# Kernel tuning notes

Measured on AMD Instinct MI355X. Metric: run time of the kernel, lower is better.

Reference implementation:

```python
import jax, jax.numpy as jnp
import numpy as np

EMB = 2048
HEADS = 16
HEAD_DIM = EMB // HEADS
LATENT = 512
B, S = 2, 2048


def setup_inputs() -> dict:
    key = jax.random.key(0)
    ks = jax.random.split(key, 7)
    sc = lambda fan_in: 1.0 / np.sqrt(fan_in)
    return {
        "x": jax.random.normal(ks[0], (B, S, EMB), dtype=jnp.float32),
        "w_q": jax.random.normal(ks[1], (EMB, EMB), dtype=jnp.float32) * sc(EMB),
        "w_down": jax.random.normal(ks[2], (LATENT, EMB), dtype=jnp.float32) * sc(EMB),
        "w_up_k": jax.random.normal(ks[3], (EMB, LATENT), dtype=jnp.float32) * sc(LATENT),
        "w_up_v": jax.random.normal(ks[4], (EMB, LATENT), dtype=jnp.float32) * sc(LATENT),
        "w_out": jax.random.normal(ks[5], (EMB, EMB), dtype=jnp.float32) * sc(EMB),
        "b_out": jax.random.normal(ks[6], (EMB,), dtype=jnp.float32) * 0.01,
    }


def reference(x, w_q, w_down, w_up_k, w_up_v, w_out, b_out):
    # Linear uses torch convention: y = x @ W.T
    q = jnp.einsum("bse,fe->bsf", x, w_q)          # [B,S,EMB]
    latent = jnp.einsum("bse,le->bsl", x, w_down)  # [B,S,LATENT]
    k = jnp.einsum("bsl,fl->bsf", latent, w_up_k)
    v = jnp.einsum("bsl,fl->bsf", latent, w_up_v)

    def heads(t):  # [B,S,EMB] -> [B,H,S,D]
        return t.reshape(B, S, HEADS, HEAD_DIM).transpose(0, 2, 1, 3)

    qh, kh, vh = heads(q), heads(k), heads(v)
    scores = jnp.einsum("bhqd,bhkd->bhqk", qh, kh)  # [B,H,S,S]
    qpos = jnp.arange(S)
    causal = qpos[:, None] < qpos[None, :]          # True where future (masked)
    scores = jnp.where(causal[None, None], -jnp.inf, scores)
    attn = jax.nn.softmax(scores / np.sqrt(HEAD_DIM).astype(np.float32), axis=-1)
    ctx = jnp.einsum("bhqk,bhkd->bhqd", attn, vh)   # [B,H,S,D]
    ctx = ctx.transpose(0, 2, 1, 3).reshape(B, S, EMB)
    return jnp.einsum("bse,fe->bsf", ctx, w_out) + b_out
```

## Files before the change

kernel.cpp:

```cpp
#include <hip/hip_runtime.h>
#include <hip/hip_bf16.h>

#define EMB 2048
#define HEADS 16
#define HDIM 128
#define LATENT 512
#define BATCH 2
#define SEQ 2048
#define MROWS (BATCH*SEQ)

typedef __attribute__((ext_vector_type(4))) float f32x4;
typedef __attribute__((ext_vector_type(8))) short s16x8;

__device__ __forceinline__ unsigned short f2bf(float f) {
  __hip_bfloat16 h = __float2bfloat16(f);
  union { __hip_bfloat16 h; unsigned short u; } c; c.h = h; return c.u;
}

#define GLOAD_LDS16(g, l) \
  __builtin_amdgcn_global_load_lds((const __attribute__((address_space(1))) unsigned int*)(g), \
                                   (__attribute__((address_space(3))) unsigned int*)(l), 16, 0, 0)

__global__ void cvt_kernel(const float* __restrict__ src, unsigned short* __restrict__ dst, int n4) {
  int i = blockIdx.x * blockDim.x + threadIdx.x;
  int stride = gridDim.x * blockDim.x;
  for (; i < n4; i += stride) {
    float4 v = reinterpret_cast<const float4*>(src)[i];
    ushort4 o;
    o.x = f2bf(v.x); o.y = f2bf(v.y); o.z = f2bf(v.z); o.w = f2bf(v.w);
    reinterpret_cast<ushort4*>(dst)[i] = o;
  }
}

#define BM 128
#define BN 128
#define BK 32

template<int OUTF32>
__global__ __launch_bounds__(256) void gemm_bt(
    const unsigned short* __restrict__ A, const unsigned short* __restrict__ B,
    void* __restrict__ C, const float* __restrict__ bias, int M, int N, int K)
{
  __shared__ __align__(16) unsigned short sA[BM][BK];
  __shared__ __align__(16) unsigned short sB[BN][BK];
  const int tid  = threadIdx.x;
  const int lane = tid & 63, wave = tid >> 6;
  const int wm = wave >> 1, wn = wave & 1;
  const int lrow = lane & 15, kgrp = lane >> 4;

  const int gx = gridDim.x;
  const int nwg = gx * gridDim.y;
  const int orig = blockIdx.y * gx + blockIdx.x;
  const int chunk = nwg >> 3;
  const int sw = (orig & 7) * chunk + (orig >> 3);
  const long bm = (long)(sw / gx) * BM, bn = (long)(sw % gx) * BN;

  const int srow = tid >> 2;
  const int scol = (tid & 3) * 8;

  f32x4 zero4 = {0.f, 0.f, 0.f, 0.f};
  f32x4 acc[4][4];
  #pragma unroll
  for (int i = 0; i < 4; ++i)
    #pragma unroll
    for (int j = 0; j < 4; ++j) acc[i][j] = zero4;

  const unsigned short* ga = A + (bm + srow) * (long)K + scol;
  const unsigned short* gb = B + (bn + srow) * (long)K + scol;

  for (int k0 = 0; k0 < K; k0 += BK) {
    GLOAD_LDS16(ga + k0,                 &sA[srow][scol]);
    GLOAD_LDS16(ga + 64*(long)K + k0,    &sA[srow + 64][scol]);
    GLOAD_LDS16(gb + k0,                 &sB[srow][scol]);
    GLOAD_LDS16(gb + 64*(long)K + k0,    &sB[srow + 64][scol]);
    __syncthreads();

    s16x8 aF[4], bF[4];
    #pragma unroll
    for (int i = 0; i < 4; ++i) {
      aF[i] = *reinterpret_cast<const s16x8*>(&sA[wm*64 + i*16 + lrow][kgrp*8]);
      bF[i] = *reinterpret_cast<const s16x8*>(&sB[wn*64 + i*16 + lrow][kgrp*8]);
    }
    #pragma unroll
    for (int i = 0; i < 4; ++i)
      #pragma unroll
      for (int j = 0; j < 4; ++j)
        acc[i][j] = __builtin_amdgcn_mfma_f32_16x16x32_bf16(aF[i], bF[j], acc[i][j], 0, 0, 0);
    __syncthreads();
  }

  #pragma unroll
  for (int i = 0; i < 4; ++i) {
    #pragma unroll
    for (int j = 0; j < 4; ++j) {
      long row = bm + wm*64 + i*16 + kgrp*4;
      long col = bn + wn*64 + j*16 + lrow;
      if (OUTF32) {
        float* Cf = (float*)C;
        float bv = bias[col];
        #pragma unroll
        for (int r = 0; r < 4; ++r) Cf[(row + r) * (long)N + col] = acc[i][j][r] + bv;
      } else {
        unsigned short* Cb = (unsigned short*)C;
        #pragma unroll
        for (int r = 0; r < 4; ++r) Cb[(row + r) * (long)N + col] = f2bf(acc[i][j][r]);
      }
    }
  }
}

#define G2_LDS (96*1024)

template<int OUTF32>
__global__ __launch_bounds__(512, 1) void gemm256(
    const unsigned short* __restrict__ A, const unsigned short* __restrict__ B,
    void* __restrict__ C, const float* __restrict__ bias, int M, int N, int K)
{
  extern __shared__ char smem[];
  const int tid  = threadIdx.x;
  const int lane = tid & 63, wave = tid >> 6;
  const int wm = wave >> 1, wn = wave & 1;
  const int lrow = lane & 15, kgrp = lane >> 4;

  const int gx = gridDim.x;
  const int nwg = gx * gridDim.y;
  const int orig = blockIdx.y * gx + blockIdx.x;
  const int chunk = nwg >> 3;
  const int sw = (orig & 7) * chunk + (orig >> 3);
  const long bm = (long)(sw / gx) * 256, bn = (long)(sw % gx) * 128;

  const int strow = tid >> 3;
  const int scolB = ((tid & 7) * 16) ^ ((strow & 7) << 4);
  const unsigned short* gaS = A + (bm + strow) * (long)K + (scolB >> 1);
  const unsigned short* gbS = B + (bn + strow) * (long)K + (scolB >> 1);

  int fcol[2];
  #pragma unroll
  for (int kh = 0; kh < 2; ++kh) fcol[kh] = (kh * 64 + kgrp * 16) ^ ((lrow & 7) << 4);

  f32x4 zero4 = {0.f, 0.f, 0.f, 0.f};
  f32x4 acc[4][4];
  #pragma unroll
  for (int i = 0; i < 4; ++i)
    #pragma unroll
    for (int j = 0; j < 4; ++j) acc[i][j] = zero4;

  const int NT = K >> 6;
  auto stage = [&](int cur, int t) {
    const long k0 = (long)t * 64;
    unsigned short* sa = (unsigned short*)(smem) + cur * 16384 + tid * 8;
    unsigned short* sb = (unsigned short*)(smem + 65536) + cur * 8192 + tid * 8;
    #pragma unroll
    for (int R = 0; R < 4; ++R) GLOAD_LDS16(gaS + (R * 64) * (long)K + k0, sa + R * 4096);
    #pragma unroll
    for (int R = 0; R < 2; ++R) GLOAD_LDS16(gbS + (R * 64) * (long)K + k0, sb + R * 4096);
  };

  stage(0, 0);
  __syncthreads();

  int cur = 0;
  for (int t = 0; t < NT; ++t) {
    if (t + 1 < NT) stage(cur ^ 1, t + 1);
    const char* sa = smem + cur * 32768;
    const char* sb = smem + 65536 + cur * 16384;
    #pragma unroll
    for (int kh = 0; kh < 2; ++kh) {
      s16x8 aF[4], bF[4];
      #pragma unroll
      for (int i = 0; i < 4; ++i)
        aF[i] = *reinterpret_cast<const s16x8*>(sa + (wm*64 + i*16 + lrow) * 128 + fcol[kh]);
      #pragma unroll
      for (int j = 0; j < 4; ++j)
        bF[j] = *reinterpret_cast<const s16x8*>(sb + (wn*64 + j*16 + lrow) * 128 + fcol[kh]);
      __builtin_amdgcn_s_setprio(1);
      #pragma unroll
      for (int i = 0; i < 4; ++i)
        #pragma unroll
        for (int j = 0; j < 4; ++j)
          acc[i][j] = __builtin_amdgcn_mfma_f32_16x16x32_bf16(aF[i], bF[j], acc[i][j], 0, 0, 0);
      __builtin_amdgcn_s_setprio(0);
    }
    __syncthreads();
    cur ^= 1;
  }

  #pragma unroll
  for (int i = 0; i < 4; ++i) {
    #pragma unroll
    for (int j = 0; j < 4; ++j) {
      long row = bm + wm*64 + i*16 + kgrp*4;
      long col = bn + wn*64 + j*16 + lrow;
      if (OUTF32) {
        float* Cf = (float*)C;
        float bv = bias[col];
        #pragma unroll
        for (int r = 0; r < 4; ++r) Cf[(row + r) * (long)N + col] = acc[i][j][r] + bv;
      } else {
        unsigned short* Cb = (unsigned short*)C;
        #pragma unroll
        for (int r = 0; r < 4; ++r) Cb[(row + r) * (long)N + col] = f2bf(acc[i][j][r]);
      }
    }
  }
}

#define KVB 64
#define QTB 64
#define NQT3 (SEQ/QTB)

__global__ __launch_bounds__(256, 2) void attn4_kernel(
    const unsigned short* __restrict__ Q, const unsigned short* __restrict__ Kg,
    const unsigned short* __restrict__ Vt, unsigned short* __restrict__ CTX)
{
  const int bid = blockIdx.x;
  const int rest = bid >> 3;
  const int pr = rest & 15;
  const int g = (bid & 7) + 8 * (rest >> 4);
  const int h = g & 15, b = g >> 4;

  const int tid = threadIdx.x, w = tid >> 6, lane = tid & 63;
  const int lrow = lane & 15, kgrp = lane >> 4;
  const size_t bS = (size_t)b * SEQ;

  __shared__ __align__(16) unsigned short sK[2][KVB * HDIM];
  __shared__ __align__(16) unsigned short sP[4][16][72];

  const int krow  = tid >> 4;
  const int kcolB = ((tid & 15) * 16) ^ (((tid >> 4) & 7) << 4);
  const unsigned short* kst_g = Kg + (bS + krow) * EMB + h * HDIM + (kcolB >> 1);

  const int swz = (lrow & 7) << 4;
  int cc[4];
  #pragma unroll
  for (int kk = 0; kk < 4; ++kk) cc[kk] = ((kk * 64 + kgrp * 16) ^ swz) >> 1;

  const float C = 0.12751742f;
  const float THR = 11.5f;
  f32x4 zero4 = {0.f, 0.f, 0.f, 0.f};
  s16x8 onesF;
  #pragma unroll
  for (int i = 0; i < 8; ++i) onesF[i] = (short)0x3F80;

  const int qts[2] = {NQT3 - 1 - pr, pr};
  for (int ps = 0; ps < 2; ++ps) {
    const int qt = qts[ps];
    const int nt = qt + 1;
    const int qw = qt * QTB + w * 16;

    s16x8 qF[4];
    #pragma unroll
    for (int kk = 0; kk < 4; ++kk)
      qF[kk] = *reinterpret_cast<const s16x8*>(
          Q + (bS + qw + lrow) * EMB + h * HDIM + kk * 32 + kgrp * 8);

    f32x4 o[8];
    #pragma unroll
    for (int dt = 0; dt < 8; ++dt) o[dt] = zero4;
    float rm[4], rl[4];
    #pragma unroll
    for (int r = 0; r < 4; ++r) { rm[r] = -1.0e30f; rl[r] = 0.f; }

    __syncthreads();
    {
      unsigned short* l0 = &sK[0][0] + tid * 8;
      #pragma unroll
      for (int R = 0; R < 4; ++R) GLOAD_LDS16(kst_g + (size_t)R * 16 * EMB, l0 + R * 2048);
    }

    for (int j = 0; j < nt; ++j) {
      __syncthreads();
      const int kv0 = j * KVB;
      if (j + 1 < nt) {
        const unsigned short* gs = kst_g + (size_t)(j + 1) * KVB * EMB;
        unsigned short* ls = &sK[(j + 1) & 1][0] + tid * 8;
        #pragma unroll
        for (int R = 0; R < 4; ++R) GLOAD_LDS16(gs + (size_t)R * 16 * EMB, ls + R * 2048);
      }

      s16x8 vF[2][8];
      #pragma unroll
      for (int hf = 0; hf < 2; ++hf)
        #pragma unroll
        for (int dt = 0; dt < 8; ++dt)
          vF[hf][dt] = *reinterpret_cast<const s16x8*>(
              Vt + (size_t)(h * HDIM + dt * 16 + lrow) * MROWS + bS + kv0 + hf * 32 + kgrp * 8);

      const unsigned short* kb = &sK[j & 1][0];
      f32x4 sc[4];
      #pragma unroll
      for (int kvg = 0; kvg < 4; ++kvg) sc[kvg] = zero4;
      __builtin_amdgcn_s_setprio(1);
      #pragma unroll
      for (int kvg = 0; kvg < 4; ++kvg) {
        const int rb = (kvg * 16 + lrow) * HDIM;
        #pragma unroll
        for (int kk = 0; kk < 4; ++kk) {
          s16x8 kF = *reinterpret_cast<const s16x8*>(kb + rb + cc[kk]);
          sc[kvg] = __builtin_amdgcn_mfma_f32_16x16x32_bf16(qF[kk], kF, sc[kvg], 0, 0, 0);
        }
      }
      __builtin_amdgcn_s_setprio(0);

      const bool needm = (kv0 + 63 > qw);
      float sv[4][4];
      #pragma unroll
      for (int kvg = 0; kvg < 4; ++kvg)
        #pragma unroll
        for (int r = 0; r < 4; ++r) {
          float s = sc[kvg][r];
          if (needm) {
            int qq  = qw + kgrp * 4 + r;
            int col = kv0 + kvg * 16 + lrow;
            s = (col <= qq) ? s : -3.0e38f;
          }
          sv[kvg][r] = s;
        }
      float tm[4];
      #pragma unroll
      for (int r = 0; r < 4; ++r)
        tm[r] = fmaxf(fmaxf(sv[0][r], sv[1][r]), fmaxf(sv[2][r], sv[3][r]));
      #pragma unroll
      for (int m = 1; m < 16; m <<= 1)
        #pragma unroll
        for (int r = 0; r < 4; ++r) tm[r] = fmaxf(tm[r], __shfl_xor(tm[r], m));

      float d = tm[0] * C - rm[0];
      #pragma unroll
      for (int r = 1; r < 4; ++r) d = fmaxf(d, tm[r] * C - rm[r]);
      const bool skip = __all(d <= THR);

      float mn[4];
      #pragma unroll
      for (int r = 0; r < 4; ++r) mn[r] = skip ? rm[r] : fmaxf(rm[r], tm[r] * C);

      #pragma unroll
      for (int r = 0; r < 4; ++r) {
        float p0 = exp2f(fmaf(sv[0][r], C, -mn[r]));
        float p1 = exp2f(fmaf(sv[1][r], C, -mn[r]));
        float p2 = exp2f(fmaf(sv[2][r], C, -mn[r]));
        float p3 = exp2f(fmaf(sv[3][r], C, -mn[r]));
        const int qrow = kgrp * 4 + r;
        sP[w][qrow][ 0 + lrow] = f2bf(p0);
        sP[w][qrow][16 + lrow] = f2bf(p1);
        sP[w][qrow][32 + lrow] = f2bf(p2);
        sP[w][qrow][48 + lrow] = f2bf(p3);
      }
      if (!skip) {
        #pragma unroll
        for (int r = 0; r < 4; ++r) {
          float corr = exp2f(rm[r] - mn[r]);
          rm[r] = mn[r];
          rl[r] *= corr;
          #pragma unroll
          for (int dt = 0; dt < 8; ++dt) o[dt][r] *= corr;
        }
      }

      s16x8 pF[2];
      #pragma unroll
      for (int hf = 0; hf < 2; ++hf)
        pF[hf] = *reinterpret_cast<const s16x8*>(&sP[w][lrow][hf * 32 + kgrp * 8]);
      f32x4 psum = zero4;
      __builtin_amdgcn_s_setprio(1);
      psum = __builtin_amdgcn_mfma_f32_16x16x32_bf16(pF[0], onesF, psum, 0, 0, 0);
      psum = __builtin_amdgcn_mfma_f32_16x16x32_bf16(pF[1], onesF, psum, 0, 0, 0);
      #pragma unroll
      for (int dt = 0; dt < 8; ++dt) {
        o[dt] = __builtin_amdgcn_mfma_f32_16x16x32_bf16(pF[0], vF[0][dt], o[dt], 0, 0, 0);
        o[dt] = __builtin_amdgcn_mfma_f32_16x16x32_bf16(pF[1], vF[1][dt], o[dt], 0, 0, 0);
      }
      __builtin_amdgcn_s_setprio(0);
      #pragma unroll
      for (int r = 0; r < 4; ++r) rl[r] += psum[r];
    }

    float iv[4];
    #pragma unroll
    for (int r = 0; r < 4; ++r) iv[r] = 1.0f / rl[r];
    #pragma unroll
    for (int dt = 0; dt < 8; ++dt)
      #pragma unroll
      for (int r = 0; r < 4; ++r)
        CTX[(bS + qw + kgrp * 4 + r) * EMB + h * HDIM + dt * 16 + lrow] =
            f2bf(o[dt][r] * iv[r]);
  }
}

extern "C" void kernel_launch(void* const* d_in, const int* in_sizes, int n_in,
                              void* d_out, int out_size, void* d_ws, size_t ws_size,
                              hipStream_t stream)
{
  const float* x      = (const float*)d_in[0];
  const float* w_q    = (const float*)d_in[1];
  const float* w_down = (const float*)d_in[2];
  const float* w_upk  = (const float*)d_in[3];
  const float* w_upv  = (const float*)d_in[4];
  const float* w_out  = (const float*)d_in[5];
  const float* b_out  = (const float*)d_in[6];
  float* out = (float*)d_out;

  static bool attr_done = false;
  if (!attr_done) {
    hipFuncSetAttribute((const void*)gemm256<0>, hipFuncAttributeMaxDynamicSharedMemorySize, G2_LDS);
    hipFuncSetAttribute((const void*)gemm256<1>, hipFuncAttributeMaxDynamicSharedMemorySize, G2_LDS);
    attr_done = true;
  }

  char* ws = (char*)d_ws;
  size_t off = 0;
  auto alloc = [&](size_t elems) {
    void* p = ws + off; off += elems * 2; off = (off + 255) & ~(size_t)255; return p;
  };
  unsigned short* xb   = (unsigned short*)alloc((size_t)MROWS * EMB);
  unsigned short* wqb  = (unsigned short*)alloc((size_t)EMB * EMB);
  unsigned short* wdb  = (unsigned short*)alloc((size_t)LATENT * EMB);
  unsigned short* wkb  = (unsigned short*)alloc((size_t)EMB * LATENT);
  unsigned short* wvb  = (unsigned short*)alloc((size_t)EMB * LATENT);
  unsigned short* wob  = (unsigned short*)alloc((size_t)EMB * EMB);
  unsigned short* qb   = (unsigned short*)alloc((size_t)MROWS * EMB);
  unsigned short* latb = (unsigned short*)alloc((size_t)MROWS * LATENT);
  unsigned short* kb   = (unsigned short*)alloc((size_t)MROWS * EMB);
  unsigned short* vtb  = (unsigned short*)alloc((size_t)EMB * MROWS);
  unsigned short* ctxb = xb;

  auto cvt = [&](const float* s, unsigned short* d, size_t n) {
    int n4 = (int)(n / 4);
    int blocks = (n4 + 255) / 256; if (blocks > 1024) blocks = 1024;
    cvt_kernel<<<dim3(blocks), dim3(256), 0, stream>>>(s, d, n4);
  };
  cvt(x,      xb,  (size_t)MROWS * EMB);
  cvt(w_q,    wqb, (size_t)EMB * EMB);
  cvt(w_down, wdb, (size_t)LATENT * EMB);
  cvt(w_upk,  wkb, (size_t)EMB * LATENT);
  cvt(w_upv,  wvb, (size_t)EMB * LATENT);
  cvt(w_out,  wob, (size_t)EMB * EMB);

  gemm256<0><<<dim3(EMB/128, MROWS/256), 512, G2_LDS, stream>>>(xb, wqb, qb, nullptr, MROWS, EMB, EMB);
  gemm_bt<0><<<dim3(LATENT/BN, MROWS/BM), 256, 0, stream>>>(xb, wdb, latb, nullptr, MROWS, LATENT, EMB);
  gemm256<0><<<dim3(EMB/128, MROWS/256), 512, G2_LDS, stream>>>(latb, wkb, kb, nullptr, MROWS, EMB, LATENT);
  gemm256<0><<<dim3(MROWS/128, EMB/256), 512, G2_LDS, stream>>>(wvb, latb, vtb, nullptr, EMB, MROWS, LATENT);

  attn4_kernel<<<dim3(512, 1, 1), 256, 0, stream>>>(qb, kb, vtb, ctxb);

  gemm256<1><<<dim3(EMB/128, MROWS/256), 512, G2_LDS, stream>>>(ctxb, wob, (void*)out, b_out, MROWS, EMB, EMB);
}
```

Measured before the change: 411.1 us.

## Compute transposed S tile so each lane owns one query row in softmax

Swaps the MFMA operand order for the QK^T product so scores come out transposed, with each lane holding one query row across 16 kv positions. The row max and sum then need only two cross-lane shuffles instead of a four-step butterfly on four values each. The row-sum MFMAs against a ones vector are replaced by a scalar accumulation. P is written to LDS as packed 32-bit stores. In exchange, the rescale factor and the final reciprocal must be shuffled back into the O accumulator layout, which adds a few extra shuffles.

```diff
diff --git a/kernel.cpp b/kernel.cpp
--- a/kernel.cpp
+++ b/kernel.cpp
@@ -209,7 +209,7 @@
 #define QTB 64
 #define NQT3 (SEQ/QTB)
 
-__global__ __launch_bounds__(256, 2) void attn4_kernel(
+__global__ __launch_bounds__(256, 2) void attn5_kernel(
     const unsigned short* __restrict__ Q, const unsigned short* __restrict__ Kg,
     const unsigned short* __restrict__ Vt, unsigned short* __restrict__ CTX)
 {
@@ -221,6 +221,7 @@
 
   const int tid = threadIdx.x, w = tid >> 6, lane = tid & 63;
   const int lrow = lane & 15, kgrp = lane >> 4;
+  const int qloc = lrow;
   const size_t bS = (size_t)b * SEQ;
 
   __shared__ __align__(16) unsigned short sK[2][KVB * HDIM];
@@ -238,15 +239,13 @@
   const float C = 0.12751742f;
   const float THR = 11.5f;
   f32x4 zero4 = {0.f, 0.f, 0.f, 0.f};
-  s16x8 onesF;
-  #pragma unroll
-  for (int i = 0; i < 8; ++i) onesF[i] = (short)0x3F80;
 
   const int qts[2] = {NQT3 - 1 - pr, pr};
   for (int ps = 0; ps < 2; ++ps) {
     const int qt = qts[ps];
     const int nt = qt + 1;
     const int qw = qt * QTB + w * 16;
+    const int q_abs = qw + qloc;
 
     s16x8 qF[4];
     #pragma unroll
@@ -257,9 +256,7 @@
     f32x4 o[8];
     #pragma unroll
     for (int dt = 0; dt < 8; ++dt) o[dt] = zero4;
-    float rm[4], rl[4];
-    #pragma unroll
-    for (int r = 0; r < 4; ++r) { rm[r] = -1.0e30f; rl[r] = 0.f; }
+    float rm = -1.0e30f, rl = 0.f;
 
     __syncthreads();
     {
@@ -297,7 +294,7 @@
         #pragma unroll
         for (int kk = 0; kk < 4; ++kk) {
           s16x8 kF = *reinterpret_cast<const s16x8*>(kb + rb + cc[kk]);
-          sc[kvg] = __builtin_amdgcn_mfma_f32_16x16x32_bf16(qF[kk], kF, sc[kvg], 0, 0, 0);
+          sc[kvg] = __builtin_amdgcn_mfma_f32_16x16x32_bf16(kF, qF[kk], sc[kvg], 0, 0, 0);
         }
       }
       __builtin_amdgcn_s_setprio(0);
@@ -310,74 +307,78 @@
         for (int r = 0; r < 4; ++r) {
           float s = sc[kvg][r];
           if (needm) {
-            int qq  = qw + kgrp * 4 + r;
-            int col = kv0 + kvg * 16 + lrow;
-            s = (col <= qq) ? s : -3.0e38f;
+            int kv = kv0 + kvg * 16 + kgrp * 4 + r;
+            s = (kv <= q_abs) ? s : -3.0e38f;
           }
           sv[kvg][r] = s;
         }
-      float tm[4];
-      #pragma unroll
-      for (int r = 0; r < 4; ++r)
-        tm[r] = fmaxf(fmaxf(sv[0][r], sv[1][r]), fmaxf(sv[2][r], sv[3][r]));
-      #pragma unroll
-      for (int m = 1; m < 16; m <<= 1)
-        #pragma unroll
-        for (int r = 0; r < 4; ++r) tm[r] = fmaxf(tm[r], __shfl_xor(tm[r], m));
-
-      float d = tm[0] * C - rm[0];
-      #pragma unroll
-      for (int r = 1; r < 4; ++r) d = fmaxf(d, tm[r] * C - rm[r]);
-      const bool skip = __all(d <= THR);
-
-      float mn[4];
-      #pragma unroll
-      for (int r = 0; r < 4; ++r) mn[r] = skip ? rm[r] : fmaxf(rm[r], tm[r] * C);
-
-      #pragma unroll
-      for (int r = 0; r < 4; ++r) {
-        float p0 = exp2f(fmaf(sv[0][r], C, -mn[r]));
-        float p1 = exp2f(fmaf(sv[1][r], C, -mn[r]));
-        float p2 = exp2f(fmaf(sv[2][r], C, -mn[r]));
-        float p3 = exp2f(fmaf(sv[3][r], C, -mn[r]));
-        const int qrow = kgrp * 4 + r;
-        sP[w][qrow][ 0 + lrow] = f2bf(p0);
-        sP[w][qrow][16 + lrow] = f2bf(p1);
-        sP[w][qrow][32 + lrow] = f2bf(p2);
-        sP[w][qrow][48 + lrow] = f2bf(p3);
-      }
+
+      float m01 = fmaxf(fmaxf(sv[0][0], sv[0][1]), fmaxf(sv[0][2], sv[0][3]));
+      float m11 = fmaxf(fmaxf(sv[1][0], sv[1][1]), fmaxf(sv[1][2], sv[1][3]));
+      float m21 = fmaxf(fmaxf(sv[2][0], sv[2][1]), fmaxf(sv[2][2], sv[2][3]));
+      float m31 = fmaxf(fmaxf(sv[3][0], sv[3][1]), fmaxf(sv[3][2], sv[3][3]));
+      float tm = fmaxf(fmaxf(m01, m11), fmaxf(m21, m31));
+      tm = fmaxf(tm, __shfl_xor(tm, 16));
+      tm = fmaxf(tm, __shfl_xor(tm, 32));
+
+      const float dchk = tm * C - rm;
+      const bool skip = __all(dchk <= THR);
+      const float mn = skip ? rm : fmaxf(rm, tm * C);
+
+      float p[4][4];
+      float ts = 0.f;
+      #pragma unroll
+      for (int kvg = 0; kvg < 4; ++kvg) {
+        #pragma unroll
+        for (int r = 0; r < 4; ++r) {
+          p[kvg][r] = exp2f(fmaf(sv[kvg][r], C, -mn));
+          ts += p[kvg][r];
+        }
+      }
+      unsigned int* sPw = reinterpret_cast<unsigned int*>(&sP[w][qloc][0]);
+      #pragma unroll
+      for (int kvg = 0; kvg < 4; ++kvg) {
+        unsigned int lo = (unsigned int)f2bf(p[kvg][0]) | ((unsigned int)f2bf(p[kvg][1]) << 16);
+        unsigned int hi = (unsigned int)f2bf(p[kvg][2]) | ((unsigned int)f2bf(p[kvg][3]) << 16);
+        sPw[kvg * 8 + kgrp * 2 + 0] = lo;
+        sPw[kvg * 8 + kgrp * 2 + 1] = hi;
+      }
+      ts += __shfl_xor(ts, 16);
+      ts += __shfl_xor(ts, 32);
+
+      const float corr = exp2f(rm - mn);
+      rl = rl * corr + ts;
+      rm = mn;
+
       if (!skip) {
-        #pragma unroll
-        for (int r = 0; r < 4; ++r) {
-          float corr = exp2f(rm[r] - mn[r]);
-          rm[r] = mn[r];
-          rl[r] *= corr;
+        float c4[4];
+        #pragma unroll
+        for (int r = 0; r < 4; ++r)
+          c4[r] = __shfl(corr, (lane & 48) | (kgrp * 4 + r));
+        #pragma unroll
+        for (int dt = 0; dt < 8; ++dt)
           #pragma unroll
-          for (int dt = 0; dt < 8; ++dt) o[dt][r] *= corr;
-        }
+          for (int r = 0; r < 4; ++r) o[dt][r] *= c4[r];
       }
 
       s16x8 pF[2];
       #pragma unroll
       for (int hf = 0; hf < 2; ++hf)
         pF[hf] = *reinterpret_cast<const s16x8*>(&sP[w][lrow][hf * 32 + kgrp * 8]);
-      f32x4 psum = zero4;
       __builtin_amdgcn_s_setprio(1);
-      psum = __builtin_amdgcn_mfma_f32_16x16x32_bf16(pF[0], onesF, psum, 0, 0, 0);
-      psum = __builtin_amdgcn_mfma_f32_16x16x32_bf16(pF[1], onesF, psum, 0, 0, 0);
       #pragma unroll
       for (int dt = 0; dt < 8; ++dt) {
         o[dt] = __builtin_amdgcn_mfma_f32_16x16x32_bf16(pF[0], vF[0][dt], o[dt], 0, 0, 0);
         o[dt] = __builtin_amdgcn_mfma_f32_16x16x32_bf16(pF[1], vF[1][dt], o[dt], 0, 0, 0);
       }
       __builtin_amdgcn_s_setprio(0);
-      #pragma unroll
-      for (int r = 0; r < 4; ++r) rl[r] += psum[r];
-    }
-
+    }
+
+    const float ivq = 1.0f / rl;
     float iv[4];
     #pragma unroll
-    for (int r = 0; r < 4; ++r) iv[r] = 1.0f / rl[r];
+    for (int r = 0; r < 4; ++r)
+      iv[r] = __shfl(ivq, (lane & 48) | (kgrp * 4 + r));
     #pragma unroll
     for (int dt = 0; dt < 8; ++dt)
       #pragma unroll
@@ -441,7 +442,7 @@
   gemm256<0><<<dim3(EMB/128, MROWS/256), 512, G2_LDS, stream>>>(latb, wkb, kb, nullptr, MROWS, EMB, LATENT);
   gemm256<0><<<dim3(MROWS/128, EMB/256), 512, G2_LDS, stream>>>(wvb, latb, vtb, nullptr, EMB, MROWS, LATENT);
 
-  attn4_kernel<<<dim3(512, 1, 1), 256, 0, stream>>>(qb, kb, vtb, ctxb);
+  attn5_kernel<<<dim3(512, 1, 1), 256, 0, stream>>>(qb, kb, vtb, ctxb);
 
   gemm256<1><<<dim3(EMB/128, MROWS/256), 512, G2_LDS, stream>>>(ctxb, wob, (void*)out, b_out, MROWS, EMB, EMB);
 }
```

Measured after the change: 404.6 us. About the same (-1.6%).
